# Performance work log

Hardware: AMD Instinct MI355X
Metric: run time of the kernel (lower is better)

Reference implementation:

```python
import jax, jax.numpy as jnp
import numpy as np

N = 50000
E = 800000
HID = 32
HEADS = 8
OUT_DIM = 16
NEG_SLOPE = 0.2
LN_EPS = 1e-5


def setup_inputs() -> dict:
    key = jax.random.key(0)
    ks = jax.random.split(key, 32)
    rn = lambda k, shape, s=0.1: (jax.random.normal(k, shape, jnp.float32) * s)
    d = {}
    d['x'] = jax.random.normal(ks[0], (N, 1), jnp.float32)
    d['edge_index'] = jax.random.randint(ks[1], (2, E), 0, N, dtype=jnp.int64)
    d['batch'] = jnp.zeros((N,), dtype=jnp.int64)
    # in_layer: Linear(1, HID)
    d['Win'] = rn(ks[2], (1, HID)); d['bin_'] = rn(ks[3], (HID,))
    # layer 0: residual Linear(HID, HID*HEADS), GATConv(HID -> HID, heads=HEADS, concat)
    d['Wr0'] = rn(ks[4], (HID, HID * HEADS)); d['br0'] = rn(ks[5], (HID * HEADS,))
    d['W0'] = rn(ks[6], (HID, HID * HEADS))
    d['as0'] = rn(ks[7], (HEADS, HID)); d['ad0'] = rn(ks[8], (HEADS, HID))
    d['bg0'] = rn(ks[9], (HID * HEADS,))
    d['g0'] = jnp.ones((HID * HEADS,), jnp.float32); d['b0'] = jnp.zeros((HID * HEADS,), jnp.float32)
    # layer 1: residual Linear(HID*HEADS, HID), GATConv(HID*HEADS -> HID, heads=1, concat=False)
    d['Wr1'] = rn(ks[10], (HID * HEADS, HID)); d['br1'] = rn(ks[11], (HID,))
    d['W1'] = rn(ks[12], (HID * HEADS, HID))
    d['as1'] = rn(ks[13], (1, HID)); d['ad1'] = rn(ks[14], (1, HID))
    d['bg1'] = rn(ks[15], (HID,))
    d['g1'] = jnp.ones((HID,), jnp.float32); d['b1'] = jnp.zeros((HID,), jnp.float32)
    # out_layer: Linear(HID, OUT_DIM)
    d['Wout'] = rn(ks[16], (HID, OUT_DIM)); d['bout'] = rn(ks[17], (OUT_DIM,))
    return d


def _layer_norm(x, g, b):
    m = x.mean(-1, keepdims=True)
    v = ((x - m) ** 2).mean(-1, keepdims=True)
    return (x - m) * jax.lax.rsqrt(v + LN_EPS) * g + b


def _gat_conv(x, src, dst, W, att_src, att_dst, bias, heads, n):
    # x: [n, in]; W: [in, heads*out]; att_*: [heads, out]
    h = (x @ W).reshape(n, heads, -1)                      # [n, H, F]
    a_s = (h * att_src).sum(-1)                            # [n, H]
    a_d = (h * att_dst).sum(-1)                            # [n, H]
    e = jax.nn.leaky_relu(a_s[src] + a_d[dst], NEG_SLOPE)  # [E', H]
    emax = jax.ops.segment_max(e, dst, num_segments=n)
    ex = jnp.exp(e - emax[dst])
    denom = jax.ops.segment_sum(ex, dst, num_segments=n)
    alpha = ex / (denom[dst] + 1e-16)                      # segment softmax per dst node
    out = jax.ops.segment_sum(h[src] * alpha[..., None], dst, num_segments=n)  # [n, H, F]
    return out.reshape(n, -1) + bias                       # concat heads (heads=1 -> mean=identity)


def reference(x, edge_index, batch, Win, bin_, Wr0, br0, W0, as0, ad0, bg0, g0, b0,
              Wr1, br1, W1, as1, ad1, bg1, g1, b1, Wout, bout):
    n = x.shape[0]
    loop = jnp.arange(n, dtype=edge_index.dtype)
    src = jnp.concatenate([edge_index[0], loop])  # PyG GATConv add_self_loops=True
    dst = jnp.concatenate([edge_index[1], loop])

    h = x @ Win + bin_                                       # [n, HID]
    # layer 0
    res = h @ Wr0 + br0
    h = _gat_conv(h, src, dst, W0, as0, ad0, bg0, HEADS, n)  # [n, HID*HEADS]
    h = jax.nn.elu(h)                                        # not last layer
    h = _layer_norm(h + res, g0, b0)
    # layer 1 (last)
    res = h @ Wr1 + br1
    h = _gat_conv(h, src, dst, W1, as1, ad1, bg1, 1, n)      # [n, HID]
    h = _layer_norm(h + res, g1, b1)
    # global mean pool
    n_graphs = 1
    sums = jax.ops.segment_sum(h, batch, num_segments=n_graphs)
    cnts = jax.ops.segment_sum(jnp.ones((n, 1), h.dtype), batch, num_segments=n_graphs)
    pooled = sums / cnts                                     # [1, HID]
    return pooled @ Wout + bout                              # [1, OUT_DIM]
```

## Files before the change

### kernel.cpp

```cpp
#include <hip/hip_runtime.h>
#include <hip/hip_fp16.h>
#include <math.h>

#define N_NODES 50000
#define N_EDGES 800000
#define HEADS 8
#define OUTD 16
#define NEG_SLOPE 0.2f
#define LN_EPS 1e-5f
#define NB0 196
#define NEGBIG -3.0e38f
#define PADDEG 64
#define NPOOL 64
#define SC_CHUNK 2048
#define SC_NCHUNK ((N_EDGES + SC_CHUNK - 1) / SC_CHUNK)
#define NGRAN 3125
#define NBLK_REMAP 12512

typedef _Float16 half8 __attribute__((ext_vector_type(8)));
typedef float f32x4 __attribute__((ext_vector_type(4)));

__device__ __forceinline__ int remap_base(int b, bool& ok) {
    int p = b & 7, q = b >> 3;
    int c = (q >> 2) * 8 + p;
    ok = (c < NGRAN);
    return c * 16 + (q & 3) * 4;
}

__global__ __launch_bounds__(256) void k_prep(const float* __restrict__ Win,
    const float* __restrict__ bin, const float* __restrict__ Wr0,
    const float* __restrict__ br0, const float* __restrict__ W0,
    const float* __restrict__ as0, const float* __restrict__ ad0,
    const float* __restrict__ Wr1, const float* __restrict__ W1,
    float* __restrict__ tab, float* __restrict__ tabPQRS,
    _Float16* __restrict__ wpk,
    int* __restrict__ cnt, float* __restrict__ partial) {
    const int t = threadIdx.x;
    const int bx = blockIdx.x;
    const int tid = bx * 256 + t;
    if (tid < N_NODES) cnt[tid] = 0;
    if (tid < NPOOL * 32) partial[tid] = 0.f;
    if (bx >= 1 && bx <= 64) {
        int idx = (bx - 1) * 256 + t;
        int j = idx & 7;
        int n = (idx >> 3) & 63;
        int qk = idx >> 9;
        int k = qk * 8 + j;
        float wv = (n < 32) ? Wr1[k * 32 + n] : W1[k * 32 + (n - 32)];
        wpk[idx] = (_Float16)wv;
    }
    if (bx != 0) return;
    __shared__ float sA1[256], sB1[256];
    float a0 = 0.f, b0 = 0.f, a1 = 0.f, b1 = 0.f;
#pragma unroll
    for (int k = 0; k < 32; k++) {
        float wk = Win[k], bk = bin[k];
        float wr = Wr0[k * 256 + t];
        float ww = W0[k * 256 + t];
        a0 = fmaf(wk, wr, a0); b0 = fmaf(bk, wr, b0);
        a1 = fmaf(wk, ww, a1); b1 = fmaf(bk, ww, b1);
    }
    b0 += br0[t];
    sA1[t] = a1; sB1[t] = b1;
    tab[t] = a0; tab[256 + t] = b0; tab[512 + t] = a1; tab[768 + t] = b1;
    __syncthreads();
    if (t < 8) {
        float P = 0.f, Q = 0.f, R = 0.f, S = 0.f;
        for (int c = 0; c < 32; c++) {
            float aw = sA1[t * 32 + c], bw = sB1[t * 32 + c];
            float av = as0[t * 32 + c], dv = ad0[t * 32 + c];
            P = fmaf(aw, av, P); Q = fmaf(bw, av, Q);
            R = fmaf(aw, dv, R); S = fmaf(bw, dv, S);
        }
        tabPQRS[t] = P; tabPQRS[8 + t] = Q; tabPQRS[16 + t] = R; tabPQRS[24 + t] = S;
    }
}

__global__ __launch_bounds__(256) void k_scatter(const int* __restrict__ srcA,
    const int* __restrict__ dstA, int* cnt, unsigned short* __restrict__ csrp) {
    const int phase = blockIdx.x & 7;
    const int chunk = blockIdx.x >> 3;
    const int4* __restrict__ d4p = (const int4*)dstA;
    const int f0 = chunk * (SC_CHUNK / 4) + threadIdx.x;
#pragma unroll
    for (int k = 0; k < 2; k++) {
        int f = f0 + k * 256;
        int e0 = f * 4;
        if (e0 < N_EDGES) {
            int4 dv = d4p[f];
            int dd[4] = {dv.x, dv.y, dv.z, dv.w};
#pragma unroll
            for (int u = 0; u < 4; u++) {
                int d = dd[u];
                if (((d >> 4) & 7) == phase) {
                    int p = atomicAdd(&cnt[d], 1);
                    if (p < PADDEG - 1) csrp[d * PADDEG + p] = (unsigned short)srcA[e0 + u];
                }
            }
        }
    }
}

__global__ __launch_bounds__(1024) void k_agg0f(const int* __restrict__ cnt,
    const unsigned short* __restrict__ csrp, const float* __restrict__ x,
    const float* __restrict__ tab, const float* __restrict__ tabPQRS,
    const float* __restrict__ bg0, const float* __restrict__ g0,
    const float* __restrict__ b0,
    const _Float16* __restrict__ wpk, const float* __restrict__ br1,
    const float* __restrict__ as1, const float* __restrict__ ad1,
    __half* __restrict__ res1h, __half* __restrict__ hW1h,
    float* __restrict__ a_s1, float* __restrict__ a_d1) {
    const int bid = blockIdx.x;
    if (bid >= NGRAN) return;
    const int base = bid * 16;
    const int t = threadIdx.x;
    const int wv = t >> 6, l = t & 63;
    __shared__ _Float16 hL[16 * 256];
    {
        const int i = base + wv;
        const int slot = l >> 3, h = l & 7;
        const int row = i * PADDEG;
        const int total = min(cnt[i], PADDEG - 1) + 1;
        const float xi = x[i];
        const float P = tabPQRS[h];
        const float C = tabPQRS[8 + h] + fmaf(xi, tabPQRS[16 + h], tabPQRS[24 + h]);
        float psum = 0.f, pxsum = 0.f;
#pragma unroll
        for (int k = 0; k < 8; k++) {
            int idx = slot + k * 8;
            if (idx >= total) break;
            int s = (idx == 0) ? i : (int)csrp[row + idx - 1];
            float xs = x[s];
            float e = fmaf(P, xs, C);
            e = (e > 0.f) ? e : NEG_SLOPE * e;
            float p = __expf(e);
            psum += p;
            pxsum = fmaf(p, xs, pxsum);
        }
        psum += __shfl_xor(psum, 8);   pxsum += __shfl_xor(pxsum, 8);
        psum += __shfl_xor(psum, 16);  pxsum += __shfl_xor(pxsum, 16);
        psum += __shfl_xor(psum, 32);  pxsum += __shfl_xor(pxsum, 32);
        const int hl = l >> 3;
        const float Ph  = __shfl(psum, hl);
        const float PXh = __shfl(pxsum, hl);
        const float inv = 1.f / (Ph + 1e-16f);
        const float Xh = PXh * inv;
        const float Sh = Ph * inv;
        const int c = l * 4;
        float4 A0v = *(const float4*)(tab + c);
        float4 B0v = *(const float4*)(tab + 256 + c);
        float4 A1v = *(const float4*)(tab + 512 + c);
        float4 B1v = *(const float4*)(tab + 768 + c);
        float4 bg = *(const float4*)(bg0 + c);
        float val[4];
        val[0] = fmaf(A1v.x, Xh, fmaf(B1v.x, Sh, bg.x));
        val[1] = fmaf(A1v.y, Xh, fmaf(B1v.y, Sh, bg.y));
        val[2] = fmaf(A1v.z, Xh, fmaf(B1v.z, Sh, bg.z));
        val[3] = fmaf(A1v.w, Xh, fmaf(B1v.w, Sh, bg.w));
#pragma unroll
        for (int k = 0; k < 4; k++) val[k] = (val[k] > 0.f) ? val[k] : (__expf(val[k]) - 1.f);
        val[0] += fmaf(xi, A0v.x, B0v.x);
        val[1] += fmaf(xi, A0v.y, B0v.y);
        val[2] += fmaf(xi, A0v.z, B0v.z);
        val[3] += fmaf(xi, A0v.w, B0v.w);
        float sm = val[0] + val[1] + val[2] + val[3];
#pragma unroll
        for (int o = 1; o <= 32; o <<= 1) sm += __shfl_xor(sm, o);
        float mean = sm * (1.f / 256.f);
        float d[4], vvv = 0.f;
#pragma unroll
        for (int k = 0; k < 4; k++) { d[k] = val[k] - mean; vvv = fmaf(d[k], d[k], vvv); }
#pragma unroll
        for (int o = 1; o <= 32; o <<= 1) vvv += __shfl_xor(vvv, o);
        float rstd = rsqrtf(vvv * (1.f / 256.f) + LN_EPS);
        float4 gv = *(const float4*)(g0 + c);
        float4 bv = *(const float4*)(b0 + c);
        __half2 o0 = __float22half2_rn(make_float2(fmaf(d[0] * rstd, gv.x, bv.x),
                                                   fmaf(d[1] * rstd, gv.y, bv.y)));
        __half2 o1 = __float22half2_rn(make_float2(fmaf(d[2] * rstd, gv.z, bv.z),
                                                   fmaf(d[3] * rstd, gv.w, bv.w)));
        uint2 ou;
        ou.x = *(unsigned*)&o0; ou.y = *(unsigned*)&o1;
        const int ks = (l >> 1) ^ (wv & 7);
        *(uint2*)(&hL[wv * 256 + ks * 8 + (l & 1) * 4]) = ou;
    }
    __syncthreads();
    if (t >= 64) return;
    const int q = l >> 4;
    const int col = l & 15;
    const half8* __restrict__ Bg = (const half8*)wpk;
    f32x4 c0 = {0.f, 0.f, 0.f, 0.f}, c1 = c0, c2 = c0, c3 = c0;
#pragma unroll
    for (int kt = 0; kt < 8; kt++) {
        const int ksr = (kt * 4 + q) ^ (col & 7);
        half8 a = *(const half8*)(&hL[col * 256 + ksr * 8]);
        const int bb = (kt * 4 + q) * 64 + col;
        half8 b0v = Bg[bb +  0];
        half8 b1v = Bg[bb + 16];
        half8 b2v = Bg[bb + 32];
        half8 b3v = Bg[bb + 48];
        c0 = __builtin_amdgcn_mfma_f32_16x16x32_f16(a, b0v, c0, 0, 0, 0);
        c1 = __builtin_amdgcn_mfma_f32_16x16x32_f16(a, b1v, c1, 0, 0, 0);
        c2 = __builtin_amdgcn_mfma_f32_16x16x32_f16(a, b2v, c2, 0, 0, 0);
        c3 = __builtin_amdgcn_mfma_f32_16x16x32_f16(a, b3v, c3, 0, 0, 0);
    }
    const int nodeE = base + q * 4;
    const float brv0 = br1[col], brv1 = br1[col + 16];
    const float asv0 = as1[col], asv1 = as1[col + 16];
    const float adv0 = ad1[col], adv1 = ad1[col + 16];
    float ps[4], pd[4];
#pragma unroll
    for (int r = 0; r < 4; r++) {
        int nd = nodeE + r;
        res1h[nd * 32 + col]      = __float2half(c0[r] + brv0);
        res1h[nd * 32 + col + 16] = __float2half(c1[r] + brv1);
        hW1h[nd * 32 + col]      = __float2half(c2[r]);
        hW1h[nd * 32 + col + 16] = __float2half(c3[r]);
        ps[r] = c2[r] * asv0 + c3[r] * asv1;
        pd[r] = c2[r] * adv0 + c3[r] * adv1;
    }
#pragma unroll
    for (int o = 1; o <= 8; o <<= 1) {
#pragma unroll
        for (int r = 0; r < 4; r++) {
            ps[r] += __shfl_xor(ps[r], o);
            pd[r] += __shfl_xor(pd[r], o);
        }
    }
    if (col == 0) {
#pragma unroll
        for (int r = 0; r < 4; r++) {
            int nd = nodeE + r;
            a_s1[nd] = ps[r]; a_d1[nd] = pd[r];
        }
    }
}

__global__ __launch_bounds__(256) void k_agg1(const int* __restrict__ cnt,
    const unsigned short* __restrict__ csrp, const float* __restrict__ a_s1,
    const float* __restrict__ a_d1, const __half* __restrict__ hW1h,
    const float* __restrict__ bg1, const __half* __restrict__ res1h,
    const float* __restrict__ g1, const float* __restrict__ b1,
    float* __restrict__ partial) {
    bool ok;
    const int base = remap_base(blockIdx.x, ok);
    if (!ok) return;
    const int t = threadIdx.x;
    const int w = t >> 6, l = t & 63;
    const int i = base + w;
    const int row = i * PADDEG;
    const int total = min(cnt[i], PADDEG - 1) + 1;
    const float ad = a_d1[i];
    const bool valid = (l < total);
    int sl = i;
    if (valid && l > 0) sl = (int)csrp[row + l - 1];
    float pl = 0.f;
    if (valid) {
        float e = a_s1[sl] + ad;
        e = (e > 0.f) ? e : NEG_SLOPE * e;
        pl = __expf(e);
    }
    float lsum = pl;
#pragma unroll
    for (int o = 1; o <= 32; o <<= 1) lsum += __shfl_xor(lsum, o);
    const float inv = 1.f / (lsum + 1e-16f);
    const int slot = l >> 3, u = l & 7;
    float4 acc = make_float4(0.f, 0.f, 0.f, 0.f);
    for (int idx = slot; idx < total; idx += 8) {
        int s = __shfl(sl, idx);
        float p = __shfl(pl, idx);
        uint2 uu = *(const uint2*)(hW1h + (size_t)s * 32 + u * 4);
        float2 v0 = __half22float2(*(const __half2*)&uu.x);
        float2 v1 = __half22float2(*(const __half2*)&uu.y);
        acc.x = fmaf(p, v0.x, acc.x); acc.y = fmaf(p, v0.y, acc.y);
        acc.z = fmaf(p, v1.x, acc.z); acc.w = fmaf(p, v1.y, acc.w);
    }
#pragma unroll
    for (int o = 8; o <= 32; o <<= 1) {
        acc.x += __shfl_xor(acc.x, o); acc.y += __shfl_xor(acc.y, o);
        acc.z += __shfl_xor(acc.z, o); acc.w += __shfl_xor(acc.w, o);
    }
    float4 bg = *(const float4*)(bg1 + u * 4);
    uint2 ru = *(const uint2*)(res1h + (size_t)i * 32 + u * 4);
    float2 rr0 = __half22float2(*(const __half2*)&ru.x);
    float2 rr1 = __half22float2(*(const __half2*)&ru.y);
    float4 val;
    val.x = fmaf(acc.x, inv, bg.x) + rr0.x; val.y = fmaf(acc.y, inv, bg.y) + rr0.y;
    val.z = fmaf(acc.z, inv, bg.z) + rr1.x; val.w = fmaf(acc.w, inv, bg.w) + rr1.y;
    float sm = val.x + val.y + val.z + val.w;
    sm += __shfl_xor(sm, 1); sm += __shfl_xor(sm, 2); sm += __shfl_xor(sm, 4);
    float mean = sm * (1.f / 32.f);
    float4 d;
    d.x = val.x - mean; d.y = val.y - mean; d.z = val.z - mean; d.w = val.w - mean;
    float vv = d.x * d.x + d.y * d.y + d.z * d.z + d.w * d.w;
    vv += __shfl_xor(vv, 1); vv += __shfl_xor(vv, 2); vv += __shfl_xor(vv, 4);
    float rstd = rsqrtf(vv * (1.f / 32.f) + LN_EPS);
    float4 gv = *(const float4*)(g1 + u * 4);
    float4 bv = *(const float4*)(b1 + u * 4);
    float4 outv;
    outv.x = fmaf(d.x * rstd, gv.x, bv.x); outv.y = fmaf(d.y * rstd, gv.y, bv.y);
    outv.z = fmaf(d.z * rstd, gv.z, bv.z); outv.w = fmaf(d.w * rstd, gv.w, bv.w);
    __shared__ float sp[4][32];
    if (l < 8) *(float4*)(&sp[w][u * 4]) = outv;
    __syncthreads();
    if (t < 32) {
        float s = sp[0][t] + sp[1][t] + sp[2][t] + sp[3][t];
        atomicAdd(&partial[(blockIdx.x & (NPOOL - 1)) * 32 + t], s);
    }
}

__global__ __launch_bounds__(64) void k_final(const float* __restrict__ partial,
                                              const float* __restrict__ Wout,
                                              const float* __restrict__ bout,
                                              float* __restrict__ out) {
    __shared__ float pooled[32];
    int t = threadIdx.x;
    if (t < 32) {
        float a = 0.f;
        for (int b = 0; b < NPOOL; b++) a += partial[b * 32 + t];
        pooled[t] = a * (1.f / (float)N_NODES);
    }
    __syncthreads();
    if (t < OUTD) {
        float o = bout[t];
        for (int c = 0; c < 32; c++) o = fmaf(pooled[c], Wout[c * OUTD + t], o);
        out[t] = o;
    }
}

extern "C" void kernel_launch(void* const* d_in, const int* in_sizes, int n_in,
                              void* d_out, int out_size, void* d_ws, size_t ws_size,
                              hipStream_t stream) {
    const float* x    = (const float*)d_in[0];
    const int*   eidx = (const int*)d_in[1];
    const float* Win  = (const float*)d_in[3];
    const float* bin  = (const float*)d_in[4];
    const float* Wr0  = (const float*)d_in[5];
    const float* br0  = (const float*)d_in[6];
    const float* W0   = (const float*)d_in[7];
    const float* as0  = (const float*)d_in[8];
    const float* ad0  = (const float*)d_in[9];
    const float* bg0  = (const float*)d_in[10];
    const float* g0   = (const float*)d_in[11];
    const float* b0   = (const float*)d_in[12];
    const float* Wr1  = (const float*)d_in[13];
    const float* br1  = (const float*)d_in[14];
    const float* W1   = (const float*)d_in[15];
    const float* as1  = (const float*)d_in[16];
    const float* ad1  = (const float*)d_in[17];
    const float* bg1  = (const float*)d_in[18];
    const float* g1   = (const float*)d_in[19];
    const float* b1   = (const float*)d_in[20];
    const float* Wout = (const float*)d_in[21];
    const float* bout = (const float*)d_in[22];
    float* out = (float*)d_out;

    const int* srcA = eidx;
    const int* dstA = eidx + N_EDGES;

    char* B = (char*)d_ws;
    __half* res1h = (__half*)(B + 25600000);
    _Float16* wpk = (_Float16*)(B + 28900000);
    __half* hW1h = (__half*)(B + 29600000);
    float* a_s1  = (float*)(B + 33600000);
    float* a_d1  = (float*)(B + 33900000);
    unsigned short* csrp = (unsigned short*)(B + 34200000);
    int* cnt     = (int*)(B + 40600000);
    float* partial = (float*)(B + 40900000);
    float* tab   = (float*)(B + 40910000);
    float* tabPQRS = (float*)(B + 40915000);

    k_prep<<<NB0, 256, 0, stream>>>(Win, bin, Wr0, br0, W0, as0, ad0, Wr1, W1,
                                    tab, tabPQRS, wpk, cnt, partial);
    k_scatter<<<SC_NCHUNK * 8, 256, 0, stream>>>(srcA, dstA, cnt, csrp);
    k_agg0f<<<NGRAN, 1024, 0, stream>>>(cnt, csrp, x, tab, tabPQRS, bg0, g0, b0,
                                        wpk, br1, as1, ad1,
                                        res1h, hW1h, a_s1, a_d1);
    k_agg1<<<NBLK_REMAP, 256, 0, stream>>>(cnt, csrp, a_s1, a_d1, hW1h,
                                           bg1, res1h, g1, b1, partial);
    k_final<<<1, 64, 0, stream>>>(partial, Wout, bout, out);
}
```

Baseline: 201.1 us.

## Fuse final pooling projection into agg1 via last-block counter; split MFMA across waves

```diff
diff --git a/kernel.cpp b/kernel.cpp
--- a/kernel.cpp
+++ b/kernel.cpp
@@ -16,6 +16,7 @@
 #define SC_NCHUNK ((N_EDGES + SC_CHUNK - 1) / SC_CHUNK)
 #define NGRAN 3125
 #define NBLK_REMAP 12512
+#define NBLK_LIVE 12500
 
 typedef _Float16 half8 __attribute__((ext_vector_type(8)));
 typedef float f32x4 __attribute__((ext_vector_type(4)));
@@ -38,7 +39,7 @@
     const int t = threadIdx.x;
     const int bx = blockIdx.x;
     const int tid = bx * 256 + t;
-    if (tid < N_NODES) cnt[tid] = 0;
+    if (tid <= N_NODES) cnt[tid] = 0;
     if (tid < NPOOL * 32) partial[tid] = 0.f;
     if (bx >= 1 && bx <= 64) {
         int idx = (bx - 1) * 256 + t;
@@ -185,53 +186,59 @@
         *(uint2*)(&hL[wv * 256 + ks * 8 + (l & 1) * 4]) = ou;
     }
     __syncthreads();
-    if (t >= 64) return;
+    if (wv >= 4) return;
     const int q = l >> 4;
     const int col = l & 15;
+    const int joff = wv << 4;
     const half8* __restrict__ Bg = (const half8*)wpk;
-    f32x4 c0 = {0.f, 0.f, 0.f, 0.f}, c1 = c0, c2 = c0, c3 = c0;
+    f32x4 cA = {0.f, 0.f, 0.f, 0.f}, cB = cA;
 #pragma unroll
     for (int kt = 0; kt < 8; kt++) {
         const int ksr = (kt * 4 + q) ^ (col & 7);
         half8 a = *(const half8*)(&hL[col * 256 + ksr * 8]);
         const int bb = (kt * 4 + q) * 64 + col;
-        half8 b0v = Bg[bb +  0];
-        half8 b1v = Bg[bb + 16];
-        half8 b2v = Bg[bb + 32];
-        half8 b3v = Bg[bb + 48];
-        c0 = __builtin_amdgcn_mfma_f32_16x16x32_f16(a, b0v, c0, 0, 0, 0);
-        c1 = __builtin_amdgcn_mfma_f32_16x16x32_f16(a, b1v, c1, 0, 0, 0);
-        c2 = __builtin_amdgcn_mfma_f32_16x16x32_f16(a, b2v, c2, 0, 0, 0);
-        c3 = __builtin_amdgcn_mfma_f32_16x16x32_f16(a, b3v, c3, 0, 0, 0);
+        cA = __builtin_amdgcn_mfma_f32_16x16x32_f16(a, Bg[bb + joff], cA, 0, 0, 0);
+        if (wv == 2)
+            cB = __builtin_amdgcn_mfma_f32_16x16x32_f16(a, Bg[bb + 48], cB, 0, 0, 0);
     }
     const int nodeE = base + q * 4;
-    const float brv0 = br1[col], brv1 = br1[col + 16];
-    const float asv0 = as1[col], asv1 = as1[col + 16];
-    const float adv0 = ad1[col], adv1 = ad1[col + 16];
-    float ps[4], pd[4];
-#pragma unroll
-    for (int r = 0; r < 4; r++) {
-        int nd = nodeE + r;
-        res1h[nd * 32 + col]      = __float2half(c0[r] + brv0);
-        res1h[nd * 32 + col + 16] = __float2half(c1[r] + brv1);
-        hW1h[nd * 32 + col]      = __float2half(c2[r]);
-        hW1h[nd * 32 + col + 16] = __float2half(c3[r]);
-        ps[r] = c2[r] * asv0 + c3[r] * asv1;
-        pd[r] = c2[r] * adv0 + c3[r] * adv1;
-    }
-#pragma unroll
-    for (int o = 1; o <= 8; o <<= 1) {
+    if (wv == 0) {
+        const float brv0 = br1[col];
+#pragma unroll
+        for (int r = 0; r < 4; r++)
+            res1h[(nodeE + r) * 32 + col] = __float2half(cA[r] + brv0);
+    } else if (wv == 1) {
+        const float brv1 = br1[col + 16];
+#pragma unroll
+        for (int r = 0; r < 4; r++)
+            res1h[(nodeE + r) * 32 + col + 16] = __float2half(cA[r] + brv1);
+    } else if (wv == 3) {
+#pragma unroll
+        for (int r = 0; r < 4; r++)
+            hW1h[(nodeE + r) * 32 + col + 16] = __float2half(cA[r]);
+    } else {
+        const float asv0 = as1[col], asv1 = as1[col + 16];
+        const float adv0 = ad1[col], adv1 = ad1[col + 16];
+        float ps[4], pd[4];
 #pragma unroll
         for (int r = 0; r < 4; r++) {
-            ps[r] += __shfl_xor(ps[r], o);
-            pd[r] += __shfl_xor(pd[r], o);
-        }
-    }
-    if (col == 0) {
-#pragma unroll
-        for (int r = 0; r < 4; r++) {
-            int nd = nodeE + r;
-            a_s1[nd] = ps[r]; a_d1[nd] = pd[r];
+            hW1h[(nodeE + r) * 32 + col] = __float2half(cA[r]);
+            ps[r] = cA[r] * asv0 + cB[r] * asv1;
+            pd[r] = cA[r] * adv0 + cB[r] * adv1;
+        }
+#pragma unroll
+        for (int o = 1; o <= 8; o <<= 1) {
+#pragma unroll
+            for (int r = 0; r < 4; r++) {
+                ps[r] += __shfl_xor(ps[r], o);
+                pd[r] += __shfl_xor(pd[r], o);
+            }
+        }
+        if (col == 0) {
+#pragma unroll
+            for (int r = 0; r < 4; r++) {
+                a_s1[nodeE + r] = ps[r]; a_d1[nodeE + r] = pd[r];
+            }
         }
     }
 }
@@ -241,7 +248,9 @@
     const float* __restrict__ a_d1, const __half* __restrict__ hW1h,
     const float* __restrict__ bg1, const __half* __restrict__ res1h,
     const float* __restrict__ g1, const float* __restrict__ b1,
-    float* __restrict__ partial) {
+    float* __restrict__ partial, int* __restrict__ done,
+    const float* __restrict__ Wout, const float* __restrict__ bout,
+    float* __restrict__ out) {
     bool ok;
     const int base = remap_base(blockIdx.x, ok);
     if (!ok) return;
@@ -303,29 +312,28 @@
     __shared__ float sp[4][32];
     if (l < 8) *(float4*)(&sp[w][u * 4]) = outv;
     __syncthreads();
+    if (t >= 64) return;
     if (t < 32) {
         float s = sp[0][t] + sp[1][t] + sp[2][t] + sp[3][t];
         atomicAdd(&partial[(blockIdx.x & (NPOOL - 1)) * 32 + t], s);
     }
-}
-
-__global__ __launch_bounds__(64) void k_final(const float* __restrict__ partial,
-                                              const float* __restrict__ Wout,
-                                              const float* __restrict__ bout,
-                                              float* __restrict__ out) {
-    __shared__ float pooled[32];
-    int t = threadIdx.x;
+    __threadfence();
+    int lastv = 0;
+    if (t == 0) lastv = (atomicAdd(done, 1) == NBLK_LIVE - 1) ? 1 : 0;
+    lastv = __shfl(lastv, 0);
+    if (!lastv) return;
+    float a = 0.f;
     if (t < 32) {
-        float a = 0.f;
-        for (int b = 0; b < NPOOL; b++) a += partial[b * 32 + t];
-        pooled[t] = a * (1.f / (float)N_NODES);
-    }
-    __syncthreads();
-    if (t < OUTD) {
-        float o = bout[t];
-        for (int c = 0; c < 32; c++) o = fmaf(pooled[c], Wout[c * OUTD + t], o);
-        out[t] = o;
-    }
+        for (int b = 0; b < NPOOL; b++) a += atomicAdd(&partial[b * 32 + t], 0.f);
+        a *= (1.f / (float)N_NODES);
+    }
+    float oo = (t < OUTD) ? bout[t] : 0.f;
+#pragma unroll
+    for (int c = 0; c < 32; c++) {
+        float pc = __shfl(a, c);
+        oo = fmaf(pc, Wout[c * OUTD + (t & 15)], oo);
+    }
+    if (t < OUTD) out[t] = oo;
 }
 
 extern "C" void kernel_launch(void* const* d_in, const int* in_sizes, int n_in,
@@ -369,6 +377,7 @@
     float* partial = (float*)(B + 40900000);
     float* tab   = (float*)(B + 40910000);
     float* tabPQRS = (float*)(B + 40915000);
+    int* done    = cnt + N_NODES;
 
     k_prep<<<NB0, 256, 0, stream>>>(Win, bin, Wr0, br0, W0, as0, ad0, Wr1, W1,
                                     tab, tabPQRS, wpk, cnt, partial);
@@ -377,6 +386,6 @@
                                         wpk, br1, as1, ad1,
                                         res1h, hW1h, a_s1, a_d1);
     k_agg1<<<NBLK_REMAP, 256, 0, stream>>>(cnt, csrp, a_s1, a_d1, hW1h,
-                                           bg1, res1h, g1, b1, partial);
-    k_final<<<1, 64, 0, stream>>>(partial, Wout, bout, out);
-}
+                                           bg1, res1h, g1, b1, partial,
+                                           done, Wout, bout, out);
+}
```

After: 446.3 us. 122% more time.
